# Kernel optimization log

Hardware: AMD Instinct MI355X
Metric: run time of the kernel (lower is better)

Reference implementation:

```python
import jax, jax.numpy as jnp
import numpy as np

D_MODEL = 1024
STATE_DIM = 256
BATCH = 4
SEQ_LEN = 4096


def setup_inputs() -> dict:
    key = jax.random.key(0)
    k_u, k_B, k_C = jax.random.split(key, 3)
    u = jax.random.normal(k_u, (BATCH, SEQ_LEN, D_MODEL), dtype=jnp.float32)
    # parameters (as in torch init)
    log_lambda = jnp.linspace(2.94, 4.6, STATE_DIM, dtype=jnp.float32)
    # nn.Linear weight shape is [out_features, in_features]
    B_w = jax.random.normal(k_B, (STATE_DIM, D_MODEL), dtype=jnp.float32) / np.sqrt(D_MODEL)
    C_w = jax.random.normal(k_C, (D_MODEL, STATE_DIM), dtype=jnp.float32) / np.sqrt(STATE_DIM)
    D = jnp.ones((D_MODEL,), dtype=jnp.float32)
    return {"u": u, "log_lambda": log_lambda, "B_w": B_w, "C_w": C_w, "D": D}


def reference(u, log_lambda, B_w, C_w, D):
    batch, seq_len, d = u.shape
    # Bu = B(u): [B, L, N]
    Bu = jnp.einsum("bld,nd->bln", u, B_w)
    lam = jax.nn.sigmoid(log_lambda)                     # [N]
    t = jnp.arange(seq_len, dtype=lam.dtype)
    kernel = lam[None, :] ** t[:, None]                  # [L, N]
    # next power of two >= 2*L (static)
    fft_len = 1
    while fft_len < 2 * seq_len:
        fft_len *= 2
    K_hat = jnp.fft.rfft(kernel, n=fft_len, axis=0)      # [F, N]
    Bu_hat = jnp.fft.rfft(Bu, n=fft_len, axis=1)         # [B, F, N]
    h_hat = K_hat[None, :, :] * Bu_hat
    h = jnp.fft.irfft(h_hat, n=fft_len, axis=1)[:, :seq_len, :]  # [B, L, N]
    y = jnp.einsum("bln,dn->bld", h, C_w) + D * u
    return y
```

## Files before the change

kernel.cpp:

```cpp
#include <hip/hip_runtime.h>
#include <hip/hip_bf16.h>

#define D_MODEL 1024
#define STATE_N 256
#define BATCH 4
#define SEQ_LEN 4096
#define M_TOTAL (BATCH * SEQ_LEN)
#define NCHUNK 128
#define CHUNK (SEQ_LEN / NCHUNK)

typedef __attribute__((ext_vector_type(8))) short bf16x8;
typedef __attribute__((ext_vector_type(4))) short s16x4;
typedef __attribute__((ext_vector_type(2))) short s16x2;
typedef __attribute__((ext_vector_type(4))) float f32x4;

static __device__ inline short f2bf(float f) {
    union { float f; unsigned u; } v; v.f = f;
    unsigned r = v.u + 0x7FFFu + ((v.u >> 16) & 1u);
    return (short)(r >> 16);
}
static __device__ inline float bf2f(short s) {
    union { unsigned u; float f; } v;
    v.u = ((unsigned)(unsigned short)s) << 16;
    return v.f;
}
static __device__ inline float sigmoidf(float x) { return 1.0f / (1.0f + expf(-x)); }

#define GLOAD_LDS16(gp, lp)                                                     \
    __builtin_amdgcn_global_load_lds(                                           \
        (const __attribute__((address_space(1))) void*)(gp),                    \
        (__attribute__((address_space(3))) void*)(lp), 16, 0, 0)

#define WAITVM(N) asm volatile("s_waitcnt vmcnt(" #N ")" ::: "memory")
#define WAITLGKM0 asm volatile("s_waitcnt lgkmcnt(0)" ::: "memory")
#define BARRIER() do { __builtin_amdgcn_s_barrier(); asm volatile("" ::: "memory"); } while (0)

__global__ void prep(const float* __restrict__ Bw, const float* __restrict__ Cw,
                     const float* __restrict__ ll,
                     short* __restrict__ Bwt, short* __restrict__ Cwt,
                     float* __restrict__ W) {
    const int bx = blockIdx.x, tid = threadIdx.x;
    if (bx >= 256) {
        const int i = bx - 256, n = tid;
        W[i * 256 + n] = powf(sigmoidf(ll[n]), (float)(31 - i));
        return;
    }
    const int g = bx * 256 + tid;
    const float* s; short* d;
    if (g < 32768) {
        const int col = g & 127, kc = (g >> 7) & 7, kt = (g >> 10) & 15, cb = g >> 14;
        s = Bw + (size_t)(cb * 128 + col) * D_MODEL + kt * 64 + kc * 8;
        d = Bwt + (size_t)g * 8;
    } else {
        const int h = g - 32768;
        const int col = h & 63, ksq = (h >> 6) & 7, tt = (h >> 9) & 3, cb = h >> 11;
        s = Cw + (size_t)(cb * 64 + col) * STATE_N + tt * 64 + ksq * 8;
        d = Cwt + (size_t)h * 8;
    }
    const f32x4 v0 = *(const f32x4*)s;
    const f32x4 v1 = *(const f32x4*)(s + 4);
    bf16x8 r;
    #pragma unroll
    for (int q = 0; q < 4; ++q) { r[q] = f2bf(v0[q]); r[4 + q] = f2bf(v1[q]); }
    *(bf16x8*)d = r;
}

__global__ __launch_bounds__(256, 2) void gemm1(const float* __restrict__ u,
                                                const short* __restrict__ Bwt,
                                                const float* __restrict__ W,
                                                short* __restrict__ Bu,
                                                float* __restrict__ ends) {
    __shared__ short Ash[2][64 * 64];
    __shared__ short Bsh[3][8 * 128 * 8];
    const int tid = threadIdx.x;
    const int lane = tid & 63, wave = tid >> 6;
    const int lr = lane & 15, kq = lane >> 4;
    const int wr = wave >> 1, wc = wave & 1;
    const int wg = ((blockIdx.x & 7) << 6) + (blockIdx.x >> 3);
    const int cb = wg & 1, strip = wg >> 1;
    const int m0 = strip * 64, n0 = cb * 128;

    const int a_r = tid >> 4, a_k = (tid & 15) * 4;
    const float* au = u + (size_t)m0 * D_MODEL + (size_t)a_r * D_MODEL + a_k;
    const int a_ch = (tid & 15) >> 1, a_half = (tid & 1) * 4;
    const short* bg = Bwt + (size_t)cb * 16 * 8192;

    f32x4 acc[2][4] = {};
    f32x4 ar0[4], ar1[4], ar2[4];

    #define LOADA(SET, KT)                                                       \
        do { _Pragma("unroll")                                                   \
             for (int i = 0; i < 4; ++i)                                         \
                 SET[i] = *(const f32x4*)(au + (size_t)i * 16 * D_MODEL + (KT) * 64); } while (0)
    #define WRITEA(BUF, SET)                                                     \
        do { _Pragma("unroll")                                                   \
             for (int i = 0; i < 4; ++i) {                                       \
                 const int row = i * 16 + a_r;                                   \
                 s16x4 wv;                                                       \
                 _Pragma("unroll")                                               \
                 for (int e = 0; e < 4; ++e) wv[e] = f2bf(SET[i][e]);            \
                 *(s16x4*)&Ash[BUF][(row * 8 + (a_ch ^ (row & 7))) * 8 + a_half] = wv; \
             } } while (0)
    #define STAGEB(BUF, KT)                                                      \
        do { const short* bs = bg + (size_t)(KT) * 8192;                         \
             _Pragma("unroll")                                                   \
             for (int q = 0; q < 4; ++q)                                         \
                 GLOAD_LDS16(bs + (q * 256 + tid) * 8,                           \
                             (char*)&Bsh[BUF][0] + (q * 256 + wave * 64) * 16); } while (0)

    LOADA(ar0, 0);
    WAITVM(0);
    WRITEA(0, ar0);
    STAGEB(0, 0);
    LOADA(ar1, 1);
    STAGEB(1, 1);
    LOADA(ar2, 2);
    WAITLGKM0;

    #pragma unroll
    for (int t = 0; t < 16; ++t) {
        if (t < 14)      { WAITVM(8); }
        else if (t == 14){ WAITVM(4); }
        else             { WAITVM(0); }
        BARRIER();
        if (t < 15) {
            if (((t + 1) % 3) == 0)      WRITEA((t + 1) & 1, ar0);
            else if (((t + 1) % 3) == 1) WRITEA((t + 1) & 1, ar1);
            else                         WRITEA((t + 1) & 1, ar2);
        }
        bf16x8 af[2][2], bfr[2][4];
        #pragma unroll
        for (int ks = 0; ks < 2; ++ks) {
            #pragma unroll
            for (int i = 0; i < 2; ++i) {
                const int row = wr * 32 + i * 16 + lr;
                af[ks][i] = *(const bf16x8*)&Ash[t & 1][(row * 8 + ((ks * 4 + kq) ^ (row & 7))) * 8];
            }
            #pragma unroll
            for (int j = 0; j < 4; ++j)
                bfr[ks][j] = *(const bf16x8*)&Bsh[t % 3][((ks * 4 + kq) * 128 + wc * 64 + j * 16 + lr) * 8];
        }
        if (t + 2 <= 15) STAGEB((t + 2) % 3, t + 2);
        if (t + 3 <= 15) {
            if (((t + 3) % 3) == 0)      LOADA(ar0, t + 3);
            else if (((t + 3) % 3) == 1) LOADA(ar1, t + 3);
            else                         LOADA(ar2, t + 3);
        }
        #pragma unroll
        for (int ks = 0; ks < 2; ++ks)
            #pragma unroll
            for (int i = 0; i < 2; ++i)
                #pragma unroll
                for (int j = 0; j < 4; ++j)
                    acc[i][j] = __builtin_amdgcn_mfma_f32_16x16x32_bf16(bfr[ks][j], af[ks][i], acc[i][j], 0, 0, 0);
    }
    #undef LOADA
    #undef WRITEA
    #undef STAGEB

    #pragma unroll
    for (int i = 0; i < 2; ++i) {
        const int m = m0 + wr * 32 + i * 16 + lr;
        #pragma unroll
        for (int j = 0; j < 4; ++j) {
            const int n = n0 + wc * 64 + j * 16 + kq * 4;
            s16x4 st;
            #pragma unroll
            for (int r = 0; r < 4; ++r) st[r] = f2bf(acc[i][j][r]);
            *(s16x4*)(Bu + (size_t)m * STATE_N + n) = st;
        }
    }

    float part[4][4];
    #pragma unroll
    for (int j = 0; j < 4; ++j) {
        const int nb = n0 + wc * 64 + j * 16 + kq * 4;
        const f32x4 w0 = *(const f32x4*)(W + (size_t)lr * 256 + nb);
        const f32x4 w1 = *(const f32x4*)(W + (size_t)(16 + lr) * 256 + nb);
        #pragma unroll
        for (int r = 0; r < 4; ++r)
            part[j][r] = w0[r] * acc[0][j][r] + w1[r] * acc[1][j][r];
    }
    #pragma unroll
    for (int m = 1; m <= 8; m <<= 1)
        #pragma unroll
        for (int j = 0; j < 4; ++j)
            #pragma unroll
            for (int r = 0; r < 4; ++r)
                part[j][r] += __shfl_xor(part[j][r], m, 64);
    if (lr == 0) {
        const int cg = strip * 2 + wr;
        #pragma unroll
        for (int j = 0; j < 4; ++j) {
            f32x4 e;
            #pragma unroll
            for (int r = 0; r < 4; ++r) e[r] = part[j][r];
            *(f32x4*)(ends + (size_t)cg * STATE_N + n0 + wc * 64 + j * 16 + kq * 4) = e;
        }
    }
}

__global__ __launch_bounds__(256) void gemm2(const short* __restrict__ Bu,
                                             const short* __restrict__ Cwt,
                                             const float* __restrict__ ll,
                                             const float* __restrict__ carries,
                                             const float* __restrict__ u,
                                             const float* __restrict__ Dv,
                                             float* __restrict__ y) {
    __shared__ short Ash[4][64 * 64];
    __shared__ short Bsh[4][8 * 64 * 8];
    const int tid = threadIdx.x;
    const int lane = tid & 63, wave = tid >> 6;
    const int lr = lane & 15, kq = lane >> 4;
    const int wr = wave >> 1, wc = wave & 1;
    const int wg = ((blockIdx.x & 7) << 9) + (blockIdx.x >> 3);
    const int cb = wg & 15, strip = wg >> 4;
    const int m0 = strip * 64, n0 = cb * 64;

    const int ch = tid >> 7;
    const int cp = tid & 127;
    const int st = cp >> 5;
    const int c0 = (2 * cp) & 63;
    const int scc = c0 >> 3, scw = c0 & 7;

    const float2 lraw = *(const float2*)(ll + 2 * cp);
    const float2 car2 = *(const float2*)(carries + (size_t)(strip * 2 + ch) * STATE_N + 2 * cp);

    const int aslot0 = wave * 128 + lane, aslot1 = aslot0 + 64;
    const int arow0 = aslot0 >> 3, arow1 = aslot1 >> 3;
    const int ac = lane & 7;
    const short* ag0 = Bu + (size_t)(m0 + arow0) * STATE_N + ((ac ^ (arow0 & 7)) << 3);
    const short* ag1 = Bu + (size_t)(m0 + arow1) * STATE_N + ((ac ^ (arow1 & 7)) << 3);
    const short* bg = Cwt + (size_t)cb * 4 * 8 * 64 * 8;

    #pragma unroll
    for (int t = 0; t < 4; ++t) {
        GLOAD_LDS16(ag0 + t * 64, (char*)&Ash[t][0] + aslot0 * 16);
        GLOAD_LDS16(ag1 + t * 64, (char*)&Ash[t][0] + aslot1 * 16);
    }
    #pragma unroll
    for (int t = 0; t < 4; ++t) {
        const short* bs = bg + (size_t)t * 4096;
        GLOAD_LDS16(bs + ((wave * 2 + 0) * 64 + lane) * 8,
                    (char*)&Bsh[t][0] + (wave * 128 + lane) * 16);
        GLOAD_LDS16(bs + ((wave * 2 + 1) * 64 + lane) * 8,
                    (char*)&Bsh[t][0] + (wave * 128 + 64 + lane) * 16);
    }

    WAITVM(8);
    BARRIER();

    {
        const float lam0 = sigmoidf(lraw.x), lam1 = sigmoidf(lraw.y);
        s16x2 rv[32];
        #pragma unroll
        for (int i = 0; i < 32; ++i)
            rv[i] = *(const s16x2*)&Ash[st][(ch * 32 + i) * 64 + ((scc ^ (i & 7)) << 3) + scw];
        float h0 = car2.x, h1 = car2.y;
        #pragma unroll
        for (int i = 0; i < 32; ++i) {
            h0 = fmaf(lam0, h0, bf2f(rv[i][0]));
            h1 = fmaf(lam1, h1, bf2f(rv[i][1]));
            s16x2 o; o[0] = f2bf(h0); o[1] = f2bf(h1);
            rv[i] = o;
        }
        #pragma unroll
        for (int i = 0; i < 32; ++i)
            *(s16x2*)&Ash[st][(ch * 32 + i) * 64 + ((scc ^ (i & 7)) << 3) + scw] = rv[i];
    }
    WAITLGKM0;
    BARRIER();

    f32x4 acc[2][2] = {};
    #pragma unroll
    for (int t = 0; t < 4; ++t) {
        if (t == 0)      { WAITVM(6); }
        else if (t == 1) { WAITVM(4); }
        else if (t == 2) { WAITVM(2); }
        else             { WAITVM(0); }
        BARRIER();
        bf16x8 af[2][2], bfr[2][2];
        #pragma unroll
        for (int ks = 0; ks < 2; ++ks) {
            #pragma unroll
            for (int i = 0; i < 2; ++i) {
                const int row = wr * 32 + i * 16 + lr;
                af[i][ks] = *(const bf16x8*)&Ash[t][row * 64 + ((((ks << 2) | kq) ^ (row & 7)) << 3)];
            }
            #pragma unroll
            for (int j = 0; j < 2; ++j)
                bfr[j][ks] = *(const bf16x8*)&Bsh[t][((ks << 2) | kq) * 512 + (wc * 32 + j * 16 + lr) * 8];
        }
        #pragma unroll
        for (int ks = 0; ks < 2; ++ks)
            #pragma unroll
            for (int i = 0; i < 2; ++i)
                #pragma unroll
                for (int j = 0; j < 2; ++j)
                    acc[i][j] = __builtin_amdgcn_mfma_f32_16x16x32_bf16(bfr[j][ks], af[i][ks], acc[i][j], 0, 0, 0);
    }

    #pragma unroll
    for (int i = 0; i < 2; ++i) {
        const int m = m0 + wr * 32 + i * 16 + lr;
        #pragma unroll
        for (int j = 0; j < 2; ++j) {
            const int n = n0 + wc * 32 + j * 16 + kq * 4;
            const size_t o = (size_t)m * D_MODEL + n;
            const f32x4 uv = *(const f32x4*)(u + o);
            const f32x4 dv = *(const f32x4*)(Dv + n);
            f32x4 rv;
            #pragma unroll
            for (int q = 0; q < 4; ++q) rv[q] = fmaf(dv[q], uv[q], acc[i][j][q]);
            *(f32x4*)(y + o) = rv;
        }
    }
}

__global__ void scan_carry(const float* __restrict__ ends,
                           const float* __restrict__ log_lambda,
                           float* __restrict__ carries) {
    const int n = threadIdx.x;
    const int b = blockIdx.x;
    const float lam = sigmoidf(log_lambda[n]);
    const float lamC = powf(lam, (float)CHUNK);
    float carry = 0.0f;
    #pragma unroll 16
    for (int c = 0; c < NCHUNK; ++c) {
        const size_t o = ((size_t)(b * NCHUNK + c)) * STATE_N + n;
        carries[o] = carry;
        carry = fmaf(lamC, carry, ends[o]);
    }
}

extern "C" void kernel_launch(void* const* d_in, const int* in_sizes, int n_in,
                              void* d_out, int out_size, void* d_ws, size_t ws_size,
                              hipStream_t stream) {
    const float* u  = (const float*)d_in[0];
    const float* ll = (const float*)d_in[1];
    const float* Bw = (const float*)d_in[2];
    const float* Cw = (const float*)d_in[3];
    const float* Dv = (const float*)d_in[4];
    float* y = (float*)d_out;

    char* ws = (char*)d_ws;
    size_t off = 0;
    short* Bwt = (short*)(ws + off); off += (size_t)STATE_N * D_MODEL * 2;
    short* Cwt = (short*)(ws + off); off += (size_t)D_MODEL * STATE_N * 2;
    float* W   = (float*)(ws + off); off += (size_t)32 * STATE_N * 4;
    short* Bu  = (short*)(ws + off); off += (size_t)M_TOTAL * STATE_N * 2;
    float* ends = (float*)(ws + off); off += (size_t)BATCH * NCHUNK * STATE_N * 4;
    float* carries = (float*)(ws + off);

    prep<<<288, 256, 0, stream>>>(Bw, Cw, ll, Bwt, Cwt, W);
    gemm1<<<512, 256, 0, stream>>>(u, Bwt, W, Bu, ends);
    scan_carry<<<BATCH, STATE_N, 0, stream>>>(ends, ll, carries);
    gemm2<<<4096, 256, 0, stream>>>(Bu, Cwt, ll, carries, u, Dv, y);
}
```

Measured before the change: 71.75 us.

## Load B weight fragments directly from global into registers, dropping LDS staging

Both GEMM kernels now read the pre-swizzled bf16 weight fragments straight from global memory into registers with a one-step double buffer, instead of staging them through LDS via global_load_lds. This removes the B shared-memory buffers and the vmcnt-based waits, and gemm1 now syncs with lgkmcnt(0) plus a barrier at the end of each iteration. The changes cut LDS footprint and LDS traffic, and gemm2 gets a higher occupancy hint (launch_bounds 256,4). The cost is more VGPRs and per-wave redundant global/L2 reads of the weights, which now have less latency hiding. In gemm2 the A tile loads are now fully drained before the scan starts.

```diff
diff --git a/kernel.cpp b/kernel.cpp
--- a/kernel.cpp
+++ b/kernel.cpp
@@ -31,7 +31,7 @@
         (const __attribute__((address_space(1))) void*)(gp),                    \
         (__attribute__((address_space(3))) void*)(lp), 16, 0, 0)
 
-#define WAITVM(N) asm volatile("s_waitcnt vmcnt(" #N ")" ::: "memory")
+#define WAITVM0   asm volatile("s_waitcnt vmcnt(0)" ::: "memory")
 #define WAITLGKM0 asm volatile("s_waitcnt lgkmcnt(0)" ::: "memory")
 #define BARRIER() do { __builtin_amdgcn_s_barrier(); asm volatile("" ::: "memory"); } while (0)
 
@@ -71,7 +71,6 @@
                                                 short* __restrict__ Bu,
                                                 float* __restrict__ ends) {
     __shared__ short Ash[2][64 * 64];
-    __shared__ short Bsh[3][8 * 128 * 8];
     const int tid = threadIdx.x;
     const int lane = tid & 63, wave = tid >> 6;
     const int lr = lane & 15, kq = lane >> 4;
@@ -81,12 +80,13 @@
     const int m0 = strip * 64, n0 = cb * 128;
 
     const int a_r = tid >> 4, a_k = (tid & 15) * 4;
-    const float* au = u + (size_t)m0 * D_MODEL + (size_t)a_r * D_MODEL + a_k;
+    const float* au = u + (size_t)(m0 + a_r) * D_MODEL + a_k;
     const int a_ch = (tid & 15) >> 1, a_half = (tid & 1) * 4;
     const short* bg = Bwt + (size_t)cb * 16 * 8192;
 
     f32x4 acc[2][4] = {};
     f32x4 ar0[4], ar1[4], ar2[4];
+    bf16x8 bfr[2][2][4];
 
     #define LOADA(SET, KT)                                                       \
         do { _Pragma("unroll")                                                   \
@@ -101,62 +101,56 @@
                  for (int e = 0; e < 4; ++e) wv[e] = f2bf(SET[i][e]);            \
                  *(s16x4*)&Ash[BUF][(row * 8 + (a_ch ^ (row & 7))) * 8 + a_half] = wv; \
              } } while (0)
-    #define STAGEB(BUF, KT)                                                      \
-        do { const short* bs = bg + (size_t)(KT) * 8192;                         \
-             _Pragma("unroll")                                                   \
-             for (int q = 0; q < 4; ++q)                                         \
-                 GLOAD_LDS16(bs + (q * 256 + tid) * 8,                           \
-                             (char*)&Bsh[BUF][0] + (q * 256 + wave * 64) * 16); } while (0)
+    #define LOADB(BUF, KT)                                                       \
+        do { _Pragma("unroll")                                                   \
+             for (int ks = 0; ks < 2; ++ks)                                      \
+                 _Pragma("unroll")                                               \
+                 for (int j = 0; j < 4; ++j)                                     \
+                     bfr[BUF][ks][j] = *(const bf16x8*)(bg + (size_t)(KT) * 8192 \
+                         + ((ks * 4 + kq) * 128 + wc * 64 + j * 16 + lr) * 8); } while (0)
 
     LOADA(ar0, 0);
-    WAITVM(0);
     WRITEA(0, ar0);
-    STAGEB(0, 0);
     LOADA(ar1, 1);
-    STAGEB(1, 1);
     LOADA(ar2, 2);
+    LOADB(0, 0);
     WAITLGKM0;
+    BARRIER();
 
     #pragma unroll
     for (int t = 0; t < 16; ++t) {
-        if (t < 14)      { WAITVM(8); }
-        else if (t == 14){ WAITVM(4); }
-        else             { WAITVM(0); }
-        BARRIER();
         if (t < 15) {
             if (((t + 1) % 3) == 0)      WRITEA((t + 1) & 1, ar0);
             else if (((t + 1) % 3) == 1) WRITEA((t + 1) & 1, ar1);
             else                         WRITEA((t + 1) & 1, ar2);
         }
-        bf16x8 af[2][2], bfr[2][4];
-        #pragma unroll
-        for (int ks = 0; ks < 2; ++ks) {
+        if (t + 3 <= 15) {
+            if (((t + 3) % 3) == 0)      LOADA(ar0, t + 3);
+            else if (((t + 3) % 3) == 1) LOADA(ar1, t + 3);
+            else                         LOADA(ar2, t + 3);
+        }
+        bf16x8 af[2][2];
+        #pragma unroll
+        for (int ks = 0; ks < 2; ++ks)
             #pragma unroll
             for (int i = 0; i < 2; ++i) {
                 const int row = wr * 32 + i * 16 + lr;
                 af[ks][i] = *(const bf16x8*)&Ash[t & 1][(row * 8 + ((ks * 4 + kq) ^ (row & 7))) * 8];
             }
-            #pragma unroll
-            for (int j = 0; j < 4; ++j)
-                bfr[ks][j] = *(const bf16x8*)&Bsh[t % 3][((ks * 4 + kq) * 128 + wc * 64 + j * 16 + lr) * 8];
-        }
-        if (t + 2 <= 15) STAGEB((t + 2) % 3, t + 2);
-        if (t + 3 <= 15) {
-            if (((t + 3) % 3) == 0)      LOADA(ar0, t + 3);
-            else if (((t + 3) % 3) == 1) LOADA(ar1, t + 3);
-            else                         LOADA(ar2, t + 3);
-        }
+        if (t < 15) LOADB((t + 1) & 1, t + 1);
         #pragma unroll
         for (int ks = 0; ks < 2; ++ks)
             #pragma unroll
             for (int i = 0; i < 2; ++i)
                 #pragma unroll
                 for (int j = 0; j < 4; ++j)
-                    acc[i][j] = __builtin_amdgcn_mfma_f32_16x16x32_bf16(bfr[ks][j], af[ks][i], acc[i][j], 0, 0, 0);
+                    acc[i][j] = __builtin_amdgcn_mfma_f32_16x16x32_bf16(bfr[t & 1][ks][j], af[ks][i], acc[i][j], 0, 0, 0);
+        WAITLGKM0;
+        BARRIER();
     }
     #undef LOADA
     #undef WRITEA
-    #undef STAGEB
+    #undef LOADB
 
     #pragma unroll
     for (int i = 0; i < 2; ++i) {
@@ -200,15 +194,14 @@
     }
 }
 
-__global__ __launch_bounds__(256) void gemm2(const short* __restrict__ Bu,
-                                             const short* __restrict__ Cwt,
-                                             const float* __restrict__ ll,
-                                             const float* __restrict__ carries,
-                                             const float* __restrict__ u,
-                                             const float* __restrict__ Dv,
-                                             float* __restrict__ y) {
+__global__ __launch_bounds__(256, 4) void gemm2(const short* __restrict__ Bu,
+                                                const short* __restrict__ Cwt,
+                                                const float* __restrict__ ll,
+                                                const float* __restrict__ carries,
+                                                const float* __restrict__ u,
+                                                const float* __restrict__ Dv,
+                                                float* __restrict__ y) {
     __shared__ short Ash[4][64 * 64];
-    __shared__ short Bsh[4][8 * 64 * 8];
     const int tid = threadIdx.x;
     const int lane = tid & 63, wave = tid >> 6;
     const int lr = lane & 15, kq = lane >> 4;
@@ -231,24 +224,26 @@
     const int ac = lane & 7;
     const short* ag0 = Bu + (size_t)(m0 + arow0) * STATE_N + ((ac ^ (arow0 & 7)) << 3);
     const short* ag1 = Bu + (size_t)(m0 + arow1) * STATE_N + ((ac ^ (arow1 & 7)) << 3);
-    const short* bg = Cwt + (size_t)cb * 4 * 8 * 64 * 8;
+    const short* bg = Cwt + (size_t)cb * 4096 * 4;
 
     #pragma unroll
     for (int t = 0; t < 4; ++t) {
         GLOAD_LDS16(ag0 + t * 64, (char*)&Ash[t][0] + aslot0 * 16);
         GLOAD_LDS16(ag1 + t * 64, (char*)&Ash[t][0] + aslot1 * 16);
     }
-    #pragma unroll
-    for (int t = 0; t < 4; ++t) {
-        const short* bs = bg + (size_t)t * 4096;
-        GLOAD_LDS16(bs + ((wave * 2 + 0) * 64 + lane) * 8,
-                    (char*)&Bsh[t][0] + (wave * 128 + lane) * 16);
-        GLOAD_LDS16(bs + ((wave * 2 + 1) * 64 + lane) * 8,
-                    (char*)&Bsh[t][0] + (wave * 128 + 64 + lane) * 16);
-    }
-
-    WAITVM(8);
+    WAITVM0;
     BARRIER();
+
+    bf16x8 bfr[2][2][2];
+    #define LOADB2(BUF, T)                                                       \
+        do { _Pragma("unroll")                                                   \
+             for (int ks = 0; ks < 2; ++ks)                                      \
+                 _Pragma("unroll")                                               \
+                 for (int j = 0; j < 2; ++j)                                     \
+                     bfr[BUF][ks][j] = *(const bf16x8*)(bg + (size_t)(T) * 4096  \
+                         + (((ks << 2) | kq) * 64 + wc * 32 + j * 16 + lr) * 8); } while (0)
+
+    LOADB2(0, 0);
 
     {
         const float lam0 = sigmoidf(lraw.x), lam1 = sigmoidf(lraw.y);
@@ -274,31 +269,24 @@
     f32x4 acc[2][2] = {};
     #pragma unroll
     for (int t = 0; t < 4; ++t) {
-        if (t == 0)      { WAITVM(6); }
-        else if (t == 1) { WAITVM(4); }
-        else if (t == 2) { WAITVM(2); }
-        else             { WAITVM(0); }
-        BARRIER();
-        bf16x8 af[2][2], bfr[2][2];
-        #pragma unroll
-        for (int ks = 0; ks < 2; ++ks) {
+        bf16x8 af[2][2];
+        #pragma unroll
+        for (int ks = 0; ks < 2; ++ks)
             #pragma unroll
             for (int i = 0; i < 2; ++i) {
                 const int row = wr * 32 + i * 16 + lr;
-                af[i][ks] = *(const bf16x8*)&Ash[t][row * 64 + ((((ks << 2) | kq) ^ (row & 7)) << 3)];
+                af[ks][i] = *(const bf16x8*)&Ash[t][row * 64 + ((((ks << 2) | kq) ^ (row & 7)) << 3)];
             }
-            #pragma unroll
-            for (int j = 0; j < 2; ++j)
-                bfr[j][ks] = *(const bf16x8*)&Bsh[t][((ks << 2) | kq) * 512 + (wc * 32 + j * 16 + lr) * 8];
-        }
+        if (t < 3) LOADB2((t + 1) & 1, t + 1);
         #pragma unroll
         for (int ks = 0; ks < 2; ++ks)
             #pragma unroll
             for (int i = 0; i < 2; ++i)
                 #pragma unroll
                 for (int j = 0; j < 2; ++j)
-                    acc[i][j] = __builtin_amdgcn_mfma_f32_16x16x32_bf16(bfr[j][ks], af[i][ks], acc[i][j], 0, 0, 0);
-    }
+                    acc[i][j] = __builtin_amdgcn_mfma_f32_16x16x32_bf16(bfr[t & 1][ks][j], af[ks][i], acc[i][j], 0, 0, 0);
+    }
+    #undef LOADB2
 
     #pragma unroll
     for (int i = 0; i < 2; ++i) {
```

Result: faster. 69.83 us (-2.7%).
